# Performance work log

Measured on AMD Instinct MI355X. Metric: run time of the kernel, lower is better.

The kernel has to match this reference:

```python
import jax, jax.numpy as jnp
import numpy as np

B, S, D, C = 64, 576, 768, 200


def setup_inputs() -> dict:
    key = jax.random.key(0)
    k1, k2, k3, k4 = jax.random.split(key, 4)
    return {
        "patch_tokens": jax.random.normal(k1, (B, S, D), dtype=jnp.float32),
        "class_token": jax.random.normal(k2, (B, D), dtype=jnp.float32),
        "attn_w": jax.random.normal(k3, (C, D), dtype=jnp.float32) * (1.0 / np.sqrt(D)),
        "attn_b": jnp.zeros((C,), dtype=jnp.float32),
        "gc_w": jax.random.normal(k4, (C, D), dtype=jnp.float32) * (1.0 / np.sqrt(D)),
        "gc_b": jnp.zeros((C,), dtype=jnp.float32),
        "lam": jnp.ones((1,), dtype=jnp.float32),
    }


def reference(patch_tokens, class_token, attn_w, attn_b, gc_w, gc_b, lam):
    # patch_tokens: (B,S,D). The torch module reshapes S to HxW, but the mean
    # over (H,W) equals the mean over S, so we stay in token layout.
    _, S_, D_ = patch_tokens.shape
    # Global classifier: (B,C)
    global_scores = class_token @ gc_w.T + gc_b
    # Per-class 1x1 conv == per-class linear projection over tokens: (B,C,S)
    att = jax.nn.sigmoid(
        jnp.einsum("bsd,cd->bcs", patch_tokens, attn_w) + attn_b[None, :, None]
    )
    # mean over spatial (S) then mean over channels (D):
    # mean_d mean_s (att * feat) == einsum / (S*D)
    attention_scores = jnp.einsum("bcs,bsd->bc", att, patch_tokens) / (S_ * D_)
    return global_scores + lam[0] * attention_scores
```

## Files before the change

kernel.cpp:

```cpp
#include <hip/hip_runtime.h>
#include <math.h>

#define Bsz  64
#define Ssz  576
#define Dsz  768
#define Csz  200
#define NKT  12

typedef float f32x4 __attribute__((ext_vector_type(4)));
typedef long  lx2   __attribute__((ext_vector_type(2)));

__global__ __launch_bounds__(256) void prep_w8(const float* __restrict__ W,
                                               unsigned long long* __restrict__ Wq) {
    const int i  = blockIdx.x * 256 + threadIdx.x;
    const int h  = i & 1;
    const int j  = i >> 1;
    const int l  = j & 63;
    const int r2 = j >> 6;
    const int t  = r2 % 13;
    const int kt = r2 / 13;
    const int q  = l >> 4, m = l & 15;
    const int row = t * 16 + m;
    const int col = kt * 64 + h * 32 + ((q >> 1) << 4) + ((q & 1) << 3);
    unsigned long long v = 0ull;
    if (row < Csz) {
        const float4 a = *(const float4*)(W + (size_t)row * Dsz + col);
        const float4 b = *(const float4*)(W + (size_t)row * Dsz + col + 4);
        unsigned int lo = __builtin_amdgcn_cvt_pk_fp8_f32(a.x, a.y, 0u, false);
        lo = __builtin_amdgcn_cvt_pk_fp8_f32(a.z, a.w, lo, true);
        unsigned int hi = __builtin_amdgcn_cvt_pk_fp8_f32(b.x, b.y, 0u, false);
        hi = __builtin_amdgcn_cvt_pk_fp8_f32(b.z, b.w, hi, true);
        v = ((unsigned long long)hi << 32) | (unsigned long long)lo;
    } else if (row == Csz) {
        v = 0x3838383838383838ull;
    }
    Wq[i] = v;
}

__global__ __launch_bounds__(256) void gc_kernel(
    const float* __restrict__ ct, const float* __restrict__ gw,
    const float* __restrict__ gb, float* __restrict__ out) {
    const int b    = blockIdx.x;
    const int wv   = threadIdx.x >> 6;
    const int lane = threadIdx.x & 63;
    const int c    = blockIdx.y * 4 + wv;
    const float* wr = gw + (size_t)c * Dsz + lane * 12;
    const float* cr = ct + (size_t)b * Dsz + lane * 12;
    float s = 0.f;
#pragma unroll
    for (int j = 0; j < 3; ++j) {
        const float4 w = *(const float4*)(wr + 4 * j);
        const float4 x = *(const float4*)(cr + 4 * j);
        s += w.x * x.x + w.y * x.y + w.z * x.z + w.w * x.w;
    }
#pragma unroll
    for (int off = 32; off > 0; off >>= 1) s += __shfl_down(s, off, 64);
    if (lane == 0) out[b * Csz + c] = s + gb[c];
}

__device__ __forceinline__ long cvtA(const f32x4 lo, const f32x4 hi) {
    union { long l; unsigned int u[2]; } A;
    A.u[0] = __builtin_amdgcn_cvt_pk_fp8_f32(lo.x, lo.y, 0u, false);
    A.u[0] = __builtin_amdgcn_cvt_pk_fp8_f32(lo.z, lo.w, A.u[0], true);
    A.u[1] = __builtin_amdgcn_cvt_pk_fp8_f32(hi.x, hi.y, 0u, false);
    A.u[1] = __builtin_amdgcn_cvt_pk_fp8_f32(hi.z, hi.w, A.u[1], true);
    return A.l;
}

__global__ __launch_bounds__(256, 4) void attn_kernel(
    const float* __restrict__ X,
    const unsigned char* __restrict__ Wq,
    const float* __restrict__ attn_b,
    const float* __restrict__ lam,
    float* __restrict__ out)
{
    __shared__ float sred[2][64][53];

    const int tid  = threadIdx.x;
    const int lane = tid & 63;
    const int w    = tid >> 6;
    const int m    = lane & 15;
    const int q    = lane >> 4;
    const int row0 = blockIdx.x * 16;
    const int bidx = blockIdx.x / 36;

    const float* xp = X + (size_t)(row0 + m) * Dsz + w * 192 + q * 8;
    const unsigned char* wp = Wq + lane * 16;

    f32x4 xr[12];
#pragma unroll
    for (int kk = 0; kk < 3; ++kk) {
#pragma unroll
        for (int j = 0; j < 4; ++j)
            xr[kk * 4 + j] = *(const f32x4*)(xp + kk * 64 + (j >> 1) * 32 + (j & 1) * 4);
    }

    f32x4 acc[13];
#pragma unroll
    for (int t = 0; t < 13; ++t) acc[t] = (f32x4){0.f, 0.f, 0.f, 0.f};

#pragma unroll
    for (int kk = 0; kk < 3; ++kk) {
        const int kt = 3 * w + kk;
        const long A0 = cvtA(xr[kk * 4 + 0], xr[kk * 4 + 1]);
        const long A1 = cvtA(xr[kk * 4 + 2], xr[kk * 4 + 3]);
        lx2 wfa[7];
#pragma unroll
        for (int t = 0; t < 7; ++t)
            wfa[t] = *(const lx2*)(wp + (size_t)(kt * 13 + t) * 1024);
        __builtin_amdgcn_s_setprio(1);
#pragma unroll
        for (int t = 0; t < 7; ++t) {
            acc[t] = __builtin_amdgcn_mfma_f32_16x16x32_fp8_fp8(A0, wfa[t][0], acc[t], 0, 0, 0);
            acc[t] = __builtin_amdgcn_mfma_f32_16x16x32_fp8_fp8(A1, wfa[t][1], acc[t], 0, 0, 0);
        }
        __builtin_amdgcn_s_setprio(0);
        lx2 wfb[6];
#pragma unroll
        for (int t = 0; t < 6; ++t)
            wfb[t] = *(const lx2*)(wp + (size_t)(kt * 13 + 7 + t) * 1024);
        __builtin_amdgcn_s_setprio(1);
#pragma unroll
        for (int t = 0; t < 6; ++t) {
            acc[7 + t] = __builtin_amdgcn_mfma_f32_16x16x32_fp8_fp8(A0, wfb[t][0], acc[7 + t], 0, 0, 0);
            acc[7 + t] = __builtin_amdgcn_mfma_f32_16x16x32_fp8_fp8(A1, wfb[t][1], acc[7 + t], 0, 0, 0);
        }
        __builtin_amdgcn_s_setprio(0);
    }

    if (w >= 2) {
#pragma unroll
        for (int t = 0; t < 13; ++t) {
#pragma unroll
            for (int r = 0; r < 4; ++r) sred[w - 2][lane][t * 4 + r] = acc[t][r];
        }
    }
    __syncthreads();
    if (w < 2) {
#pragma unroll
        for (int t = 0; t < 13; ++t) {
#pragma unroll
            for (int r = 0; r < 4; ++r) acc[t][r] += sred[w][lane][t * 4 + r];
        }
    }
    __syncthreads();
    if (w == 1) {
#pragma unroll
        for (int t = 0; t < 13; ++t) {
#pragma unroll
            for (int r = 0; r < 4; ++r) sred[0][lane][t * 4 + r] = acc[t][r];
        }
    }
    __syncthreads();

    if (w == 0) {
#pragma unroll
        for (int t = 0; t < 13; ++t) {
#pragma unroll
            for (int r = 0; r < 4; ++r) acc[t][r] += sred[0][lane][t * 4 + r];
        }
        float rsv[4];
#pragma unroll
        for (int r = 0; r < 4; ++r) rsv[r] = __shfl(acc[12][r], (lane & 48) + 8, 64);

        const float scale = lam[0] * (1.f / ((float)Ssz * (float)Dsz));
#pragma unroll
        for (int t = 0; t < 13; ++t) {
            const int c = t * 16 + m;
            if (c < Csz) {
                const float bias = attn_b[c];
                float s = 0.f;
#pragma unroll
                for (int r = 0; r < 4; ++r)
                    s += rsv[r] / (1.f + __expf(-(acc[t][r] + bias)));
                s += __shfl_xor(s, 16, 64);
                s += __shfl_xor(s, 32, 64);
                if (q == 0) atomicAdd(&out[bidx * Csz + c], s * scale);
            }
        }
    }
}

extern "C" void kernel_launch(void* const* d_in, const int* in_sizes, int n_in,
                              void* d_out, int out_size, void* d_ws, size_t ws_size,
                              hipStream_t stream) {
    const float* X   = (const float*)d_in[0];
    const float* ct  = (const float*)d_in[1];
    const float* aw  = (const float*)d_in[2];
    const float* ab  = (const float*)d_in[3];
    const float* gw  = (const float*)d_in[4];
    const float* gb  = (const float*)d_in[5];
    const float* lam = (const float*)d_in[6];
    float* out = (float*)d_out;
    unsigned long long* Wq = (unsigned long long*)d_ws;

    prep_w8<<<(NKT * 13 * 64 * 2) / 256, 256, 0, stream>>>(aw, Wq);
    gc_kernel<<<dim3(Bsz, Csz / 4), 256, 0, stream>>>(ct, gw, gb, out);
    attn_kernel<<<(Bsz * Ssz) / 16, 256, 0, stream>>>(X, (const unsigned char*)Wq, ab, lam, out);
}
```

Baseline: 197.0 us.

## Pre-quantize X to FP8 in MFMA fragment layout via separate kernel

Adds a separate pass that converts the fp32 patch tokens to fp8 and writes them into the MFMA fragment order in workspace. The attention kernel then loads three 16-byte fragments per lane instead of twelve fp32 vectors and converting them inline. This moves the conversion out of the MFMA kernel but adds a full extra read of X plus a write and re-read of the quantized copy, which raises total memory traffic.

```diff
diff --git a/kernel.cpp b/kernel.cpp
--- a/kernel.cpp
+++ b/kernel.cpp
@@ -6,6 +6,7 @@
 #define Dsz  768
 #define Csz  200
 #define NKT  12
+#define NRB  2304
 
 typedef float f32x4 __attribute__((ext_vector_type(4)));
 typedef long  lx2   __attribute__((ext_vector_type(2)));
@@ -37,6 +38,23 @@
     Wq[i] = v;
 }
 
+__global__ __launch_bounds__(256) void xq_kernel(const float* __restrict__ X,
+                                                 unsigned char* __restrict__ Xq) {
+    const int tid0 = blockIdx.x * 256 + threadIdx.x;
+    for (int i = tid0; i < (Bsz * Ssz * Dsz / 4); i += 2048 * 256) {
+        const float4 v = ((const float4*)X)[i];
+        unsigned int u = __builtin_amdgcn_cvt_pk_fp8_f32(v.x, v.y, 0u, false);
+        u = __builtin_amdgcn_cvt_pk_fp8_f32(v.z, v.w, u, true);
+        const int row  = i / 192;
+        const int c4   = (i - row * 192) * 4;
+        const int rblk = row >> 4, m = row & 15;
+        const int kt   = c4 >> 6,  c6 = c4 & 63;
+        const int k2   = c6 >> 5,  q = (c6 >> 3) & 3, b0 = c6 & 7;
+        *(unsigned int*)(Xq + (((size_t)rblk * 12 + kt) << 10)
+                            + (((q << 4) | m) << 4) + (k2 << 3) + b0) = u;
+    }
+}
+
 __global__ __launch_bounds__(256) void gc_kernel(
     const float* __restrict__ ct, const float* __restrict__ gw,
     const float* __restrict__ gb, float* __restrict__ out) {
@@ -58,17 +76,34 @@
     if (lane == 0) out[b * Csz + c] = s + gb[c];
 }
 
-__device__ __forceinline__ long cvtA(const f32x4 lo, const f32x4 hi) {
-    union { long l; unsigned int u[2]; } A;
-    A.u[0] = __builtin_amdgcn_cvt_pk_fp8_f32(lo.x, lo.y, 0u, false);
-    A.u[0] = __builtin_amdgcn_cvt_pk_fp8_f32(lo.z, lo.w, A.u[0], true);
-    A.u[1] = __builtin_amdgcn_cvt_pk_fp8_f32(hi.x, hi.y, 0u, false);
-    A.u[1] = __builtin_amdgcn_cvt_pk_fp8_f32(hi.z, hi.w, A.u[1], true);
-    return A.l;
+__device__ __forceinline__ void mmkk(const long A0, const long A1,
+                                     const unsigned char* wrec, f32x4 (&acc)[13]) {
+    lx2 wfa[7];
+#pragma unroll
+    for (int t = 0; t < 7; ++t)
+        wfa[t] = *(const lx2*)(wrec + (size_t)t * 1024);
+    __builtin_amdgcn_s_setprio(1);
+#pragma unroll
+    for (int t = 0; t < 7; ++t) {
+        acc[t] = __builtin_amdgcn_mfma_f32_16x16x32_fp8_fp8(A0, wfa[t][0], acc[t], 0, 0, 0);
+        acc[t] = __builtin_amdgcn_mfma_f32_16x16x32_fp8_fp8(A1, wfa[t][1], acc[t], 0, 0, 0);
+    }
+    __builtin_amdgcn_s_setprio(0);
+    lx2 wfb[6];
+#pragma unroll
+    for (int t = 0; t < 6; ++t)
+        wfb[t] = *(const lx2*)(wrec + (size_t)(7 + t) * 1024);
+    __builtin_amdgcn_s_setprio(1);
+#pragma unroll
+    for (int t = 0; t < 6; ++t) {
+        acc[7 + t] = __builtin_amdgcn_mfma_f32_16x16x32_fp8_fp8(A0, wfb[t][0], acc[7 + t], 0, 0, 0);
+        acc[7 + t] = __builtin_amdgcn_mfma_f32_16x16x32_fp8_fp8(A1, wfb[t][1], acc[7 + t], 0, 0, 0);
+    }
+    __builtin_amdgcn_s_setprio(0);
 }
 
 __global__ __launch_bounds__(256, 4) void attn_kernel(
-    const float* __restrict__ X,
+    const unsigned char* __restrict__ Xq,
     const unsigned char* __restrict__ Wq,
     const float* __restrict__ attn_b,
     const float* __restrict__ lam,
@@ -81,52 +116,23 @@
     const int w    = tid >> 6;
     const int m    = lane & 15;
     const int q    = lane >> 4;
-    const int row0 = blockIdx.x * 16;
+    const int rblk = blockIdx.x;
     const int bidx = blockIdx.x / 36;
 
-    const float* xp = X + (size_t)(row0 + m) * Dsz + w * 192 + q * 8;
+    const unsigned char* xqp = Xq + (((size_t)rblk * 12 + 3 * w) << 10) + lane * 16;
+    const lx2 xf0 = *(const lx2*)(xqp);
+    const lx2 xf1 = *(const lx2*)(xqp + 1024);
+    const lx2 xf2 = *(const lx2*)(xqp + 2048);
+
     const unsigned char* wp = Wq + lane * 16;
 
-    f32x4 xr[12];
-#pragma unroll
-    for (int kk = 0; kk < 3; ++kk) {
-#pragma unroll
-        for (int j = 0; j < 4; ++j)
-            xr[kk * 4 + j] = *(const f32x4*)(xp + kk * 64 + (j >> 1) * 32 + (j & 1) * 4);
-    }
-
     f32x4 acc[13];
 #pragma unroll
     for (int t = 0; t < 13; ++t) acc[t] = (f32x4){0.f, 0.f, 0.f, 0.f};
 
-#pragma unroll
-    for (int kk = 0; kk < 3; ++kk) {
-        const int kt = 3 * w + kk;
-        const long A0 = cvtA(xr[kk * 4 + 0], xr[kk * 4 + 1]);
-        const long A1 = cvtA(xr[kk * 4 + 2], xr[kk * 4 + 3]);
-        lx2 wfa[7];
-#pragma unroll
-        for (int t = 0; t < 7; ++t)
-            wfa[t] = *(const lx2*)(wp + (size_t)(kt * 13 + t) * 1024);
-        __builtin_amdgcn_s_setprio(1);
-#pragma unroll
-        for (int t = 0; t < 7; ++t) {
-            acc[t] = __builtin_amdgcn_mfma_f32_16x16x32_fp8_fp8(A0, wfa[t][0], acc[t], 0, 0, 0);
-            acc[t] = __builtin_amdgcn_mfma_f32_16x16x32_fp8_fp8(A1, wfa[t][1], acc[t], 0, 0, 0);
-        }
-        __builtin_amdgcn_s_setprio(0);
-        lx2 wfb[6];
-#pragma unroll
-        for (int t = 0; t < 6; ++t)
-            wfb[t] = *(const lx2*)(wp + (size_t)(kt * 13 + 7 + t) * 1024);
-        __builtin_amdgcn_s_setprio(1);
-#pragma unroll
-        for (int t = 0; t < 6; ++t) {
-            acc[7 + t] = __builtin_amdgcn_mfma_f32_16x16x32_fp8_fp8(A0, wfb[t][0], acc[7 + t], 0, 0, 0);
-            acc[7 + t] = __builtin_amdgcn_mfma_f32_16x16x32_fp8_fp8(A1, wfb[t][1], acc[7 + t], 0, 0, 0);
-        }
-        __builtin_amdgcn_s_setprio(0);
-    }
+    mmkk(xf0[0], xf0[1], wp + (size_t)(3 * w + 0) * 13 * 1024, acc);
+    mmkk(xf1[0], xf1[1], wp + (size_t)(3 * w + 1) * 13 * 1024, acc);
+    mmkk(xf2[0], xf2[1], wp + (size_t)(3 * w + 2) * 13 * 1024, acc);
 
     if (w >= 2) {
 #pragma unroll
@@ -193,8 +199,10 @@
     const float* lam = (const float*)d_in[6];
     float* out = (float*)d_out;
     unsigned long long* Wq = (unsigned long long*)d_ws;
+    unsigned char* Xq = (unsigned char*)d_ws + (1 << 20);
 
     prep_w8<<<(NKT * 13 * 64 * 2) / 256, 256, 0, stream>>>(aw, Wq);
+    xq_kernel<<<2048, 256, 0, stream>>>(X, Xq);
     gc_kernel<<<dim3(Bsz, Csz / 4), 256, 0, stream>>>(ct, gw, gb, out);
-    attn_kernel<<<(Bsz * Ssz) / 16, 256, 0, stream>>>(X, (const unsigned char*)Wq, ab, lam, out);
-}
+    attn_kernel<<<NRB, 256, 0, stream>>>(Xq, (const unsigned char*)Wq, ab, lam, out);
+}
```

Result: slower. 225.4 us (+14.4%).
